# Kernel tuning notes

Measured on AMD Instinct MI355X. Metric: run time of the kernel, lower is better.

## Reference

```python
import jax, jax.numpy as jnp
import numpy as np

N = 50000
E = 1600000
D_IN = 128
HID = 128
EPS = 1e-5
NEG_SLOPE = 0.2


def setup_inputs() -> dict:
    key = jax.random.key(0)
    ks = jax.random.split(key, 16)
    s = 1.0 / np.sqrt(D_IN)
    inp = {
        'x': jax.random.normal(ks[0], (N, D_IN), dtype=jnp.float32),
        'edge_index': jax.random.randint(ks[1], (2, E), 0, N, dtype=jnp.int64),
        # layer 0 params
        'W0': jax.random.normal(ks[2], (D_IN, HID), dtype=jnp.float32) * s,
        'att_src0': jax.random.normal(ks[3], (HID,), dtype=jnp.float32) * s,
        'att_dst0': jax.random.normal(ks[4], (HID,), dtype=jnp.float32) * s,
        'bias0': jnp.zeros((HID,), dtype=jnp.float32),
        'gamma0': jnp.ones((HID,), dtype=jnp.float32),
        'beta0': jnp.zeros((HID,), dtype=jnp.float32),
        # layer 1 params
        'W1': jax.random.normal(ks[5], (HID, HID), dtype=jnp.float32) * s,
        'att_src1': jax.random.normal(ks[6], (HID,), dtype=jnp.float32) * s,
        'att_dst1': jax.random.normal(ks[7], (HID,), dtype=jnp.float32) * s,
        'bias1': jnp.zeros((HID,), dtype=jnp.float32),
        'gamma1': jnp.ones((HID,), dtype=jnp.float32),
        'beta1': jnp.zeros((HID,), dtype=jnp.float32),
    }
    return inp


def _gat_conv(x, W, a_src, a_dst, bias, src, dst, n_nodes):
    h = x @ W                                   # [N, HID]
    alpha_src = h @ a_src                       # [N]
    alpha_dst = h @ a_dst                       # [N]
    e = jax.nn.leaky_relu(alpha_src[src] + alpha_dst[dst], NEG_SLOPE)  # [E']
    # numerically stable softmax over edges grouped by destination node
    m = jax.ops.segment_max(e, dst, num_segments=n_nodes)
    ex = jnp.exp(e - m[dst])
    denom = jax.ops.segment_sum(ex, dst, num_segments=n_nodes)
    alpha = ex / denom[dst]                     # [E']
    out = jax.ops.segment_sum(h[src] * alpha[:, None], dst, num_segments=n_nodes)
    return out + bias


def _batch_norm(x, gamma, beta):
    mean = jnp.mean(x, axis=0)
    var = jnp.mean(jnp.square(x - mean), axis=0)  # biased variance (torch BN normalization)
    return gamma * (x - mean) * jax.lax.rsqrt(var + EPS) + beta


def reference(x, edge_index, W0, att_src0, att_dst0, bias0, gamma0, beta0,
              W1, att_src1, att_dst1, bias1, gamma1, beta1):
    n = x.shape[0]
    loops = jnp.arange(n, dtype=edge_index.dtype)
    src = jnp.concatenate([edge_index[0], loops])
    dst = jnp.concatenate([edge_index[1], loops])

    h = _gat_conv(x, W0, att_src0, att_dst0, bias0, src, dst, n)
    h = _batch_norm(h, gamma0, beta0)
    h = jax.nn.relu(h)
    # dropout: identity in eval mode

    h = _gat_conv(h, W1, att_src1, att_dst1, bias1, src, dst, n)
    h = _batch_norm(h, gamma1, beta1)
    h = jax.nn.relu(h)  # last_activation=True
    return h
```

## Files before the change

kernel.cpp:

```cpp
#include <hip/hip_runtime.h>
#include <math.h>

#define HID 128
#define PAD 96
#define NB 196
#define CAP 10240
#define CHUNK 4096
#define AGG_BLOCKS 2048
#define NEG_SLOPE 0.2f
#define EPS 1e-5f

typedef __attribute__((ext_vector_type(8))) short short8;
typedef __attribute__((ext_vector_type(4))) float floatx4;

static __device__ __forceinline__ unsigned bf16_rne(float x) {
    unsigned u = __float_as_uint(x);
    return (u + 0x7fffu + ((u >> 16) & 1u)) >> 16;
}
static __device__ __forceinline__ float bf16lo_f(unsigned u) { return __uint_as_float(u << 16); }
static __device__ __forceinline__ float bf16hi_f(unsigned u) { return __uint_as_float(u & 0xffff0000u); }

__global__ void wt_build(const float* __restrict__ W, unsigned short* __restrict__ Wt,
                         unsigned short* __restrict__ Hb, int N) {
    int t = threadIdx.x;
    if (t < 64) ((unsigned*)(Hb + (size_t)N * HID))[t] = 0u;
    for (int task = t; task < 2048; task += 256) {
        int c = task & 127, k0 = (task >> 7) * 8;
        unsigned v[8];
#pragma unroll
        for (int j = 0; j < 8; ++j) v[j] = bf16_rne(W[(k0 + j) * HID + c]);
        uint4 st;
        st.x = v[0] | (v[1] << 16);
        st.y = v[2] | (v[3] << 16);
        st.z = v[4] | (v[5] << 16);
        st.w = v[6] | (v[7] << 16);
        *(uint4*)&Wt[c * HID + k0] = st;
    }
}

template <bool BN>
__global__ __launch_bounds__(256) void gemm_mfma(
    const float* __restrict__ X, const unsigned short* __restrict__ Wt,
    const float* __restrict__ a_src, const float* __restrict__ a_dst,
    const float* __restrict__ coef,
    unsigned short* __restrict__ Hb, float* __restrict__ asrc, float* __restrict__ adst,
    int N)
{
    int tid = threadIdx.x;
    int wv = tid >> 6, lane = tid & 63;
    int g = lane >> 4, c = lane & 15;
    int r0w = blockIdx.x * 64 + wv * 16;
    int arow = r0w + c;
    bool avalid = arow < N;
    const float* xr = X + (size_t)(avalid ? arow : 0) * HID;

    floatx4 acc[8];
#pragma unroll
    for (int i = 0; i < 8; ++i) acc[i] = (floatx4)0.f;

#pragma unroll
    for (int kc = 0; kc < 4; ++kc) {
        int k0 = kc * 32 + g * 8;
        float xv[8];
        float4 x0 = *(const float4*)&xr[k0];
        float4 x1 = *(const float4*)&xr[k0 + 4];
        xv[0] = x0.x; xv[1] = x0.y; xv[2] = x0.z; xv[3] = x0.w;
        xv[4] = x1.x; xv[5] = x1.y; xv[6] = x1.z; xv[7] = x1.w;
        if (BN) {
            float4 s0 = *(const float4*)&coef[k0];
            float4 s1 = *(const float4*)&coef[k0 + 4];
            float4 h0 = *(const float4*)&coef[HID + k0];
            float4 h1 = *(const float4*)&coef[HID + k0 + 4];
            xv[0] = fmaxf(fmaf(xv[0], s0.x, h0.x), 0.f);
            xv[1] = fmaxf(fmaf(xv[1], s0.y, h0.y), 0.f);
            xv[2] = fmaxf(fmaf(xv[2], s0.z, h0.z), 0.f);
            xv[3] = fmaxf(fmaf(xv[3], s0.w, h0.w), 0.f);
            xv[4] = fmaxf(fmaf(xv[4], s1.x, h1.x), 0.f);
            xv[5] = fmaxf(fmaf(xv[5], s1.y, h1.y), 0.f);
            xv[6] = fmaxf(fmaf(xv[6], s1.z, h1.z), 0.f);
            xv[7] = fmaxf(fmaf(xv[7], s1.w, h1.w), 0.f);
        }
        short8 af;
#pragma unroll
        for (int j = 0; j < 8; ++j) af[j] = avalid ? (short)bf16_rne(xv[j]) : (short)0;

#pragma unroll
        for (int nt = 0; nt < 8; ++nt) {
            short8 bf = *(const short8*)&Wt[(nt * 16 + c) * HID + k0];
            acc[nt] = __builtin_amdgcn_mfma_f32_16x16x32_bf16(af, bf, acc[nt], 0, 0, 0);
        }
    }

    float as_c[8], ad_c[8];
#pragma unroll
    for (int nt = 0; nt < 8; ++nt) {
        as_c[nt] = a_src[nt * 16 + c];
        ad_c[nt] = a_dst[nt * 16 + c];
    }
#pragma unroll
    for (int reg = 0; reg < 4; ++reg) {
        float s = 0.f, d = 0.f;
#pragma unroll
        for (int nt = 0; nt < 8; ++nt) {
            s = fmaf(acc[nt][reg], as_c[nt], s);
            d = fmaf(acc[nt][reg], ad_c[nt], d);
        }
#pragma unroll
        for (int o = 1; o < 16; o <<= 1) {
            s += __shfl_xor(s, o);
            d += __shfl_xor(d, o);
        }
        int crow = r0w + g * 4 + reg;
        if (c == 0 && crow < N) { asrc[crow] = s; adst[crow] = d; }
    }
#pragma unroll
    for (int reg = 0; reg < 4; ++reg) {
        int crow = r0w + g * 4 + reg;
        if (crow < N) {
#pragma unroll
            for (int nt = 0; nt < 8; ++nt)
                Hb[(size_t)crow * HID + nt * 16 + c] = (unsigned short)bf16_rne(acc[nt][reg]);
        }
    }
}

__global__ __launch_bounds__(256) void scatter_part(
    const int* __restrict__ ei, int* __restrict__ bcur,
    unsigned int* __restrict__ bbuf, int E)
{
    __shared__ int lcnt[NB], gbase[NB];
    int tid = threadIdx.x;
    int i0 = blockIdx.x * CHUNK;
    int i1 = i0 + CHUNK; if (i1 > E) i1 = E;
    if (tid < NB) lcnt[tid] = 0;
    __syncthreads();
    for (int i = i0 + tid; i < i1; i += 256)
        atomicAdd(&lcnt[ei[E + i] >> 8], 1);
    __syncthreads();
    if (tid < NB) {
        gbase[tid] = atomicAdd(&bcur[tid], lcnt[tid]);
        lcnt[tid] = 0;
    }
    __syncthreads();
    for (int i = i0 + tid; i < i1; i += 256) {
        int s = ei[i], d = ei[E + i];
        int b = d >> 8;
        int off = atomicAdd(&lcnt[b], 1);
        int pos = gbase[b] + off;
        if (pos < CAP)
            bbuf[(size_t)b * CAP + pos] = ((unsigned)s << 8) | (unsigned)(d & 255);
    }
}

__global__ __launch_bounds__(256) void ell_build(
    const unsigned int* __restrict__ bbuf, const int* __restrict__ bcur,
    int* __restrict__ cnt, int* __restrict__ ell, float* __restrict__ asrc, int N)
{
    __shared__ int stage[256 * PAD];
    __shared__ int scnt[256];
    int tid = threadIdx.x;
    int b = blockIdx.x;
    int base = b << 8;
    int nodes = N - base; if (nodes > 256) nodes = 256;

    if (b == 0 && tid == 0) asrc[N] = -1e30f;

    int4 s4; s4.x = s4.y = s4.z = s4.w = N;
    for (int idx = tid * 4; idx < 256 * PAD; idx += 1024)
        *(int4*)&stage[idx] = s4;
    __syncthreads();
    for (int i = tid; i < nodes; i += 256) {
        stage[i * PAD] = base + i;
        scnt[i] = 1;
    }
    __syncthreads();

    int nb = bcur[b]; if (nb > CAP) nb = CAP;
    const unsigned int* buf = bbuf + (size_t)b * CAP;
    for (int j = tid; j < nb; j += 256) {
        unsigned int v = buf[j];
        int dl = (int)(v & 255u);
        int s = (int)(v >> 8);
        int p = atomicAdd(&scnt[dl], 1);
        if (p < PAD) stage[dl * PAD + p] = s;
    }
    __syncthreads();

    int total = nodes * PAD;
    int* dst = ell + (size_t)base * PAD;
    for (int idx = tid * 4; idx < total; idx += 1024)
        *(int4*)&dst[idx] = *(const int4*)&stage[idx];
    for (int i = tid; i < nodes; i += 256)
        cnt[base + i] = scnt[i];
}

__global__ __launch_bounds__(256) void gat_aggregate(
    const unsigned short* __restrict__ Hb, const float* __restrict__ asrc,
    const float* __restrict__ adst, const int* __restrict__ cnt,
    const int* __restrict__ ell, const float* __restrict__ bias,
    float* __restrict__ OUT, float* __restrict__ stat, int N)
{
    __shared__ float sbuf[4][HID], qbuf[4][HID];
    int tid = threadIdx.x, wv = tid >> 6, lane = tid & 63;
    int c0 = 2 * lane;
    float b0 = bias[c0], b1 = bias[c0 + 1];
    float ssum0 = 0.f, ssum1 = 0.f, sq0 = 0.f, sq1 = 0.f;

    for (int n = blockIdx.x * 4 + wv; n < N; n += AGG_BLOCKS * 4) {
        int nn = __builtin_amdgcn_readfirstlane(n);
        int deg = cnt[nn]; if (deg > PAD) deg = PAD;
        const int* row = ell + (size_t)nn * PAD;
        float adn = adst[nn];
        float acc0 = 0.f, acc1 = 0.f, den = 0.f;

        for (int j = 0; j < deg; j += 8) {
            int4 sA = *(const int4*)&row[j];
            int4 sB = *(const int4*)&row[j + 4];
#define EDG(SI) { int si = (SI);                                      \
            float v = asrc[si] + adn;                                 \
            v = fmaxf(v, v * NEG_SLOPE);                              \
            float w = __expf(v);                                      \
            den += w;                                                 \
            unsigned hv = *(const unsigned*)(Hb + (size_t)si * HID + c0); \
            acc0 = fmaf(w, bf16lo_f(hv), acc0);                       \
            acc1 = fmaf(w, bf16hi_f(hv), acc1); }
            EDG(sA.x) EDG(sA.y) EDG(sA.z) EDG(sA.w)
            EDG(sB.x) EDG(sB.y) EDG(sB.z) EDG(sB.w)
#undef EDG
        }
        float inv = 1.f / den;
        float o0 = fmaf(acc0, inv, b0);
        float o1 = fmaf(acc1, inv, b1);
        *(float2*)&OUT[(size_t)nn * HID + c0] = make_float2(o0, o1);
        ssum0 += o0; ssum1 += o1;
        sq0 = fmaf(o0, o0, sq0); sq1 = fmaf(o1, o1, sq1);
    }

    sbuf[wv][c0] = ssum0; sbuf[wv][c0 + 1] = ssum1;
    qbuf[wv][c0] = sq0;   qbuf[wv][c0 + 1] = sq1;
    __syncthreads();
    if (tid < HID) {
        float t = sbuf[0][tid] + sbuf[1][tid] + sbuf[2][tid] + sbuf[3][tid];
        atomicAdd(&stat[tid], t);
    } else {
        int cc = tid - HID;
        float t = qbuf[0][cc] + qbuf[1][cc] + qbuf[2][cc] + qbuf[3][cc];
        atomicAdd(&stat[HID + cc], t);
    }
}

__global__ void bn_coef(const float* __restrict__ stat, const float* __restrict__ gamma,
                        const float* __restrict__ beta, float* __restrict__ coef,
                        float invN)
{
    int c = threadIdx.x;
    float mean = stat[c] * invN;
    float var = stat[HID + c] * invN - mean * mean;
    float s = gamma[c] * rsqrtf(var + EPS);
    coef[c] = s;
    coef[HID + c] = beta[c] - mean * s;
}

__global__ __launch_bounds__(256) void bn_apply(
    float* __restrict__ X, const float* __restrict__ coef, int N)
{
    int tid = threadIdx.x, lane = tid & 63, wv = tid >> 6;
    int c0 = 2 * lane;
    float s0 = coef[c0], s1 = coef[c0 + 1];
    float h0 = coef[HID + c0], h1 = coef[HID + c0 + 1];
    for (int r = blockIdx.x * 4 + wv; r < N; r += gridDim.x * 4) {
        float2 v = *(float2*)&X[(size_t)r * HID + c0];
        float y0 = fmaxf(fmaf(v.x, s0, h0), 0.f);
        float y1 = fmaxf(fmaf(v.y, s1, h1), 0.f);
        *(float2*)&X[(size_t)r * HID + c0] = make_float2(y0, y1);
    }
}

extern "C" void kernel_launch(void* const* d_in, const int* in_sizes, int n_in,
                              void* d_out, int out_size, void* d_ws, size_t ws_size,
                              hipStream_t stream)
{
    const float* x        = (const float*)d_in[0];
    const int*   ei       = (const int*)d_in[1];
    const float* W0       = (const float*)d_in[2];
    const float* att_src0 = (const float*)d_in[3];
    const float* att_dst0 = (const float*)d_in[4];
    const float* bias0    = (const float*)d_in[5];
    const float* gamma0   = (const float*)d_in[6];
    const float* beta0    = (const float*)d_in[7];
    const float* W1       = (const float*)d_in[8];
    const float* att_src1 = (const float*)d_in[9];
    const float* att_dst1 = (const float*)d_in[10];
    const float* bias1    = (const float*)d_in[11];
    const float* gamma1   = (const float*)d_in[12];
    const float* beta1    = (const float*)d_in[13];

    const int N = in_sizes[0] / HID;
    const int E = in_sizes[1] / 2;
    float* out = (float*)d_out;

    char* wsbase = (char*)d_ws;
    size_t off = 0;
    auto alloc = [&](size_t bytes) -> void* {
        void* p = wsbase + off;
        off += (bytes + 255) & ~(size_t)255;
        return p;
    };
    unsigned short* Hb   = (unsigned short*)alloc((size_t)(N + 1) * HID * 2);
    float*          asrc = (float*)alloc((size_t)(N + 1) * 4);
    float*          adst = (float*)alloc((size_t)N * 4);
    int*            cnt  = (int*)  alloc((size_t)N * 4);
    int*            ell  = (int*)  alloc((size_t)N * PAD * 4);
    unsigned int*   bbuf = (unsigned int*)alloc((size_t)NB * CAP * 4);
    int*            bcur = (int*)  alloc(NB * 4);
    float*          stats = (float*)alloc(4 * HID * 4);
    float*          coef0 = (float*)alloc(2 * HID * 4);
    float*          coef1 = (float*)alloc(2 * HID * 4);
    unsigned short* Wt0  = (unsigned short*)alloc(HID * HID * 2);
    unsigned short* Wt1  = (unsigned short*)alloc(HID * HID * 2);
    float* stat0 = stats;
    float* stat1 = stats + 2 * HID;

    const int gemm_blocks  = (N + 63) / 64;
    const int part_blocks  = (E + CHUNK - 1) / CHUNK;
    const int build_blocks = (N + 255) / 256;
    const float invN = 1.0f / (float)N;

    (void)hipMemsetAsync(bcur, 0, NB * 4, stream);
    (void)hipMemsetAsync(stats, 0, 4 * HID * 4, stream);

    wt_build<<<1, 256, 0, stream>>>(W0, Wt0, Hb, N);
    wt_build<<<1, 256, 0, stream>>>(W1, Wt1, Hb, N);
    scatter_part<<<part_blocks, 256, 0, stream>>>(ei, bcur, bbuf, E);
    ell_build<<<build_blocks, 256, 0, stream>>>(bbuf, bcur, cnt, ell, asrc, N);

    gemm_mfma<false><<<gemm_blocks, 256, 0, stream>>>(
        x, Wt0, att_src0, att_dst0, nullptr, Hb, asrc, adst, N);
    gat_aggregate<<<AGG_BLOCKS, 256, 0, stream>>>(
        Hb, asrc, adst, cnt, ell, bias0, out, stat0, N);
    bn_coef<<<1, HID, 0, stream>>>(stat0, gamma0, beta0, coef0, invN);

    gemm_mfma<true><<<gemm_blocks, 256, 0, stream>>>(
        out, Wt1, att_src1, att_dst1, coef0, Hb, asrc, adst, N);
    gat_aggregate<<<AGG_BLOCKS, 256, 0, stream>>>(
        Hb, asrc, adst, cnt, ell, bias1, out, stat1, N);
    bn_coef<<<1, HID, 0, stream>>>(stat1, gamma1, beta1, coef1, invN);
    bn_apply<<<2048, 256, 0, stream>>>(out, coef1, N);
}
```

Baseline: 309.1 us.

## Split wave into four edge groups with 16-byte feature loads in GAT aggregation

The aggregation kernel now splits each 64-lane wave into four quarter-waves. Each quarter-wave handles a different subset of edges, and each lane loads 8 bf16 features as one 16-byte load instead of 2 features per lane. Partial sums and denominators are combined with cross-lane shuffles before normalization and the store. This raises memory-level parallelism on the random row gathers and cuts per-edge scalar work. The cost is more registers, the shuffle reductions, and redundant softmax-weight computation spread across lanes.

After: 324.1 us. 1.05x slower.

```diff
diff --git a/kernel.cpp b/kernel.cpp
--- a/kernel.cpp
+++ b/kernel.cpp
@@ -202,42 +202,86 @@
 {
     __shared__ float sbuf[4][HID], qbuf[4][HID];
     int tid = threadIdx.x, wv = tid >> 6, lane = tid & 63;
-    int c0 = 2 * lane;
-    float b0 = bias[c0], b1 = bias[c0 + 1];
-    float ssum0 = 0.f, ssum1 = 0.f, sq0 = 0.f, sq1 = 0.f;
+    int q = lane >> 4, li = lane & 15;
+    int c0 = li * 8;
+    float b8[8];
+#pragma unroll
+    for (int i = 0; i < 8; ++i) b8[i] = bias[c0 + i];
+    float ssum[8], sq[8];
+#pragma unroll
+    for (int i = 0; i < 8; ++i) { ssum[i] = 0.f; sq[i] = 0.f; }
 
     for (int n = blockIdx.x * 4 + wv; n < N; n += AGG_BLOCKS * 4) {
         int nn = __builtin_amdgcn_readfirstlane(n);
         int deg = cnt[nn]; if (deg > PAD) deg = PAD;
         const int* row = ell + (size_t)nn * PAD;
         float adn = adst[nn];
-        float acc0 = 0.f, acc1 = 0.f, den = 0.f;
+        float acc[8];
+#pragma unroll
+        for (int i = 0; i < 8; ++i) acc[i] = 0.f;
+        float den = 0.f;
 
         for (int j = 0; j < deg; j += 8) {
-            int4 sA = *(const int4*)&row[j];
-            int4 sB = *(const int4*)&row[j + 4];
-#define EDG(SI) { int si = (SI);                                      \
-            float v = asrc[si] + adn;                                 \
-            v = fmaxf(v, v * NEG_SLOPE);                              \
-            float w = __expf(v);                                      \
-            den += w;                                                 \
-            unsigned hv = *(const unsigned*)(Hb + (size_t)si * HID + c0); \
-            acc0 = fmaf(w, bf16lo_f(hv), acc0);                       \
-            acc1 = fmaf(w, bf16hi_f(hv), acc1); }
-            EDG(sA.x) EDG(sA.y) EDG(sA.z) EDG(sA.w)
-            EDG(sB.x) EDG(sB.y) EDG(sB.z) EDG(sB.w)
-#undef EDG
+            int siA = row[j + q];
+            int siB = row[j + 4 + q];
+            float vA = asrc[siA] + adn;
+            float vB = asrc[siB] + adn;
+            vA = fmaxf(vA, vA * NEG_SLOPE);
+            vB = fmaxf(vB, vB * NEG_SLOPE);
+            float wA = __expf(vA);
+            float wB = __expf(vB);
+            uint4 hA = *(const uint4*)(Hb + (size_t)siA * HID + c0);
+            uint4 hB = *(const uint4*)(Hb + (size_t)siB * HID + c0);
+            den += wA + wB;
+            acc[0] = fmaf(wA, bf16lo_f(hA.x), acc[0]);
+            acc[1] = fmaf(wA, bf16hi_f(hA.x), acc[1]);
+            acc[2] = fmaf(wA, bf16lo_f(hA.y), acc[2]);
+            acc[3] = fmaf(wA, bf16hi_f(hA.y), acc[3]);
+            acc[4] = fmaf(wA, bf16lo_f(hA.z), acc[4]);
+            acc[5] = fmaf(wA, bf16hi_f(hA.z), acc[5]);
+            acc[6] = fmaf(wA, bf16lo_f(hA.w), acc[6]);
+            acc[7] = fmaf(wA, bf16hi_f(hA.w), acc[7]);
+            acc[0] = fmaf(wB, bf16lo_f(hB.x), acc[0]);
+            acc[1] = fmaf(wB, bf16hi_f(hB.x), acc[1]);
+            acc[2] = fmaf(wB, bf16lo_f(hB.y), acc[2]);
+            acc[3] = fmaf(wB, bf16hi_f(hB.y), acc[3]);
+            acc[4] = fmaf(wB, bf16lo_f(hB.z), acc[4]);
+            acc[5] = fmaf(wB, bf16hi_f(hB.z), acc[5]);
+            acc[6] = fmaf(wB, bf16lo_f(hB.w), acc[6]);
+            acc[7] = fmaf(wB, bf16hi_f(hB.w), acc[7]);
+        }
+
+        den += __shfl_xor(den, 16);
+        den += __shfl_xor(den, 32);
+#pragma unroll
+        for (int i = 0; i < 8; ++i) {
+            acc[i] += __shfl_xor(acc[i], 16);
+            acc[i] += __shfl_xor(acc[i], 32);
         }
         float inv = 1.f / den;
-        float o0 = fmaf(acc0, inv, b0);
-        float o1 = fmaf(acc1, inv, b1);
-        *(float2*)&OUT[(size_t)nn * HID + c0] = make_float2(o0, o1);
-        ssum0 += o0; ssum1 += o1;
-        sq0 = fmaf(o0, o0, sq0); sq1 = fmaf(o1, o1, sq1);
-    }
-
-    sbuf[wv][c0] = ssum0; sbuf[wv][c0 + 1] = ssum1;
-    qbuf[wv][c0] = sq0;   qbuf[wv][c0 + 1] = sq1;
+        float o[8];
+#pragma unroll
+        for (int i = 0; i < 8; ++i) {
+            o[i] = fmaf(acc[i], inv, b8[i]);
+            ssum[i] += o[i];
+            sq[i] = fmaf(o[i], o[i], sq[i]);
+        }
+        if (q == 0) {
+            float4 st0, st1;
+            st0.x = o[0]; st0.y = o[1]; st0.z = o[2]; st0.w = o[3];
+            st1.x = o[4]; st1.y = o[5]; st1.z = o[6]; st1.w = o[7];
+            *(float4*)&OUT[(size_t)nn * HID + c0] = st0;
+            *(float4*)&OUT[(size_t)nn * HID + c0 + 4] = st1;
+        }
+    }
+
+    if (q == 0) {
+#pragma unroll
+        for (int i = 0; i < 8; ++i) {
+            sbuf[wv][c0 + i] = ssum[i];
+            qbuf[wv][c0 + i] = sq[i];
+        }
+    }
     __syncthreads();
     if (tid < HID) {
         float t = sbuf[0][tid] + sbuf[1][tid] + sbuf[2][tid] + sbuf[3][tid];
```
